# Kernel optimization log

Hardware: AMD Instinct MI355X
Metric: run time of the kernel (lower is better)

The kernel has to match this reference:

```python
import jax, jax.numpy as jnp
import numpy as np

B, N, E, H = 64, 2048, 256, 256


def _scan_dir(xproj, Whh, bhh, reverse):
    # xproj: (B, N, H) precomputed input projection; recurrence h_t = tanh(xproj_t + h @ Whh.T + bhh)
    def step(h, xt):
        h = jnp.tanh(xt + h @ Whh.T + bhh)
        return h, h
    h0 = jnp.zeros((xproj.shape[0], Whh.shape[0]), xproj.dtype)
    _, seq = jax.lax.scan(step, h0, jnp.swapaxes(xproj, 0, 1), reverse=reverse)
    return jnp.swapaxes(seq, 0, 1)  # (B, N, H)


def _bilayer(inp, Wf, bf, Uf, cf, Wb, bb, Ub, cb):
    fore = _scan_dir(inp @ Wf.T + bf, Uf, cf, False)
    back = _scan_dir(inp @ Wb.T + bb, Ub, cb, True)
    return jnp.concatenate([fore, back], axis=-1), fore[:, -1, :], back[:, 0, :]


def setup_inputs() -> dict:
    key = jax.random.key(0)
    ks = jax.random.split(key, 17)
    s_e = 1.0 / np.sqrt(E)
    s_h = 1.0 / np.sqrt(H)
    s_2h = 1.0 / np.sqrt(2 * H)
    f32 = jnp.float32
    return {
        'x': jax.random.normal(ks[0], (B, N, E), f32),
        'Wih_f0': jax.random.normal(ks[1], (H, E), f32) * s_e,
        'bih_f0': jax.random.normal(ks[2], (H,), f32) * s_e,
        'Whh_f0': jax.random.normal(ks[3], (H, H), f32) * s_h,
        'bhh_f0': jax.random.normal(ks[4], (H,), f32) * s_h,
        'Wih_b0': jax.random.normal(ks[5], (H, E), f32) * s_e,
        'bih_b0': jax.random.normal(ks[6], (H,), f32) * s_e,
        'Whh_b0': jax.random.normal(ks[7], (H, H), f32) * s_h,
        'bhh_b0': jax.random.normal(ks[8], (H,), f32) * s_h,
        'Wih_f1': jax.random.normal(ks[9], (H, 2 * H), f32) * s_2h,
        'bih_f1': jax.random.normal(ks[10], (H,), f32) * s_2h,
        'Whh_f1': jax.random.normal(ks[11], (H, H), f32) * s_h,
        'bhh_f1': jax.random.normal(ks[12], (H,), f32) * s_h,
        'Wih_b1': jax.random.normal(ks[13], (H, 2 * H), f32) * s_2h,
        'bih_b1': jax.random.normal(ks[14], (H,), f32) * s_2h,
        'Whh_b1': jax.random.normal(ks[15], (H, H), f32) * s_h,
        'bhh_b1': jax.random.normal(ks[16], (H,), f32) * s_h,
    }


def reference(x, Wih_f0, bih_f0, Whh_f0, bhh_f0, Wih_b0, bih_b0, Whh_b0, bhh_b0,
              Wih_f1, bih_f1, Whh_f1, bhh_f1, Wih_b1, bih_b1, Whh_b1, bhh_b1):
    out0, _, _ = _bilayer(x, Wih_f0, bih_f0, Whh_f0, bhh_f0, Wih_b0, bih_b0, Whh_b0, bhh_b0)
    _, h_f, h_b = _bilayer(out0, Wih_f1, bih_f1, Whh_f1, bhh_f1, Wih_b1, bih_b1, Whh_b1, bhh_b1)
    return jnp.concatenate([h_f, h_b], axis=-1)  # (B, 2H) final hidden of last layer
```

## Files before the change

### kernel.cpp

```cpp
#include <hip/hip_runtime.h>

#define BATCH 64
#define SEQ   2048
#define EIN   256
#define HID   256

typedef _Float16 f16;
typedef _Float16 f16x8 __attribute__((ext_vector_type(8)));
typedef float    f32x4 __attribute__((ext_vector_type(4)));

__global__ __launch_bounds__(256) void cast_f32_f16(
    const float* __restrict__ s, f16* __restrict__ d, int n)
{
    int i = (blockIdx.x * 256 + threadIdx.x) * 8;
    if (i >= n) return;
    const float4* sp = reinterpret_cast<const float4*>(s + i);
    float4 a = sp[0], b = sp[1];
    f16x8 v = { (f16)a.x, (f16)a.y, (f16)a.z, (f16)a.w,
                (f16)b.x, (f16)b.y, (f16)b.z, (f16)b.w };
    *reinterpret_cast<f16x8*>(d + i) = v;
}

__global__ __launch_bounds__(256, 2) void gemm_proj(
    const f16* __restrict__ A, const f16* __restrict__ W,
    const float* __restrict__ bias, f16* __restrict__ C, int K)
{
    const int tid  = threadIdx.x;
    const int wave = tid >> 6, lane = tid & 63;
    const int g    = lane >> 4, lr = lane & 15;
    const int bm   = blockIdx.x * 128;
    const int bn   = blockIdx.y * 128;
    const int wm   = (wave >> 1) * 64, wn = (wave & 1) * 64;

    __shared__ __align__(16) f16 As[128][72];
    __shared__ __align__(16) f16 Bs[128][72];

    f32x4 acc[4][4] = {};

    for (int kt = 0; kt < K; kt += 64) {
        __syncthreads();
#pragma unroll
        for (int i = 0; i < 4; ++i) {
            int c = i * 256 + tid;
            int r = c >> 3, sg = c & 7;
            *reinterpret_cast<f16x8*>(&As[r][sg * 8]) =
                *reinterpret_cast<const f16x8*>(A + (size_t)(bm + r) * K + kt + sg * 8);
            *reinterpret_cast<f16x8*>(&Bs[r][sg * 8]) =
                *reinterpret_cast<const f16x8*>(W + (size_t)(bn + r) * K + kt + sg * 8);
        }
        __syncthreads();
#pragma unroll
        for (int kf = 0; kf < 2; ++kf) {
            f16x8 af[4], bf[4];
#pragma unroll
            for (int f = 0; f < 4; ++f) {
                af[f] = *reinterpret_cast<const f16x8*>(&As[wm + f * 16 + lr][kf * 32 + g * 8]);
                bf[f] = *reinterpret_cast<const f16x8*>(&Bs[wn + f * 16 + lr][kf * 32 + g * 8]);
            }
#pragma unroll
            for (int fm = 0; fm < 4; ++fm)
#pragma unroll
                for (int fn = 0; fn < 4; ++fn)
                    acc[fm][fn] = __builtin_amdgcn_mfma_f32_16x16x32_f16(
                        af[fm], bf[fn], acc[fm][fn], 0, 0, 0);
        }
    }

#pragma unroll
    for (int fn = 0; fn < 4; ++fn) {
        float bv = bias[bn + wn + fn * 16 + lr];
#pragma unroll
        for (int fm = 0; fm < 4; ++fm) {
#pragma unroll
            for (int i = 0; i < 4; ++i) {
                int row = bm + wm + fm * 16 + g * 4 + i;
                int col = bn + wn + fn * 16 + lr;
                C[(size_t)row * 256 + col] = (f16)(acc[fm][fn][i] + bv);
            }
        }
    }
}

template<bool WRITE_SEQ>
__global__ __launch_bounds__(256, 1) void rnn_scan(
    const f16* __restrict__ xpF, const f16* __restrict__ xpB,
    const float* __restrict__ WhhF, const float* __restrict__ bhhF,
    const float* __restrict__ WhhB, const float* __restrict__ bhhB,
    f16* __restrict__ seq_out,
    float* __restrict__ fin_out)
{
    const int blk = blockIdx.x;
    const int b   = blk >> 1, dir = blk & 1;
    const f16*   xp  = dir ? xpB : xpF;
    const float* Whh = dir ? WhhB : WhhF;
    const float* bhh = dir ? bhhB : bhhF;

    const int tid  = threadIdx.x;
    const int wave = tid >> 6, lane = tid & 63;
    const int g    = lane >> 4, lr = lane & 15;
    const int n0   = wave * 64;

    __shared__ __align__(16) f16 hbuf[2][256];

    int kfj[8];
#pragma unroll
    for (int j = 0; j < 8; ++j) kfj[j] = (2 * wave + j) & 7;

    f16x8 wf[4][8];
#pragma unroll
    for (int fn = 0; fn < 4; ++fn) {
        const float* wr = Whh + (size_t)(n0 + fn * 16 + lr) * 256;
#pragma unroll
        for (int j = 0; j < 8; ++j) {
            const float4* p = reinterpret_cast<const float4*>(wr + kfj[j] * 32 + g * 8);
            float4 x0 = p[0], x1 = p[1];
            wf[fn][j] = (f16x8){ (f16)x0.x, (f16)x0.y, (f16)x0.z, (f16)x0.w,
                                 (f16)x1.x, (f16)x1.y, (f16)x1.z, (f16)x1.w };
        }
    }
    const float bv = bhh[tid];

    int aoff[8];
#pragma unroll
    for (int j = 0; j < 8; ++j) aoff[j] = kfj[j] * 64 + g * 16;
    char* lds0 = (char*)&hbuf[0][0];
    char* lds1 = (char*)&hbuf[1][0];

    hbuf[0][tid] = (f16)0.f;
    __syncthreads();

    const long long xstep = dir ? -256 : 256;
    const f16* xpre;
    {
        const f16* xptr = xp + (long long)b * SEQ * 256
                             + (long long)(dir ? SEQ - 1 : 0) * 256 + tid;
        xpre = xptr;
    }
    const long long sstep = dir ? -512 : 512;
    f16* sptr = nullptr;
    if (WRITE_SEQ)
        sptr = seq_out + ((long long)b * SEQ + (dir ? SEQ - 1 : 0)) * 512 + dir * 256 + tid;

    f16 ring[4];
#pragma unroll
    for (int r = 0; r < 3; ++r) { ring[r] = *xpre; xpre += xstep; }

    const f32x4 zf = {0.f, 0.f, 0.f, 0.f};
    float last_h = 0.f;

    f16x8 af[8];
    af[0] = *reinterpret_cast<const f16x8*>(lds0 + aoff[0]);
    af[1] = *reinterpret_cast<const f16x8*>(lds0 + aoff[1]);

    for (int s4 = 0; s4 < SEQ; s4 += 4) {
#pragma unroll
        for (int u = 0; u < 4; ++u) {
            char* cur = (u & 1) ? lds1 : lds0;
            char* nxt = (u & 1) ? lds0 : lds1;

#pragma unroll
            for (int j = 2; j < 8; ++j)
                af[j] = *reinterpret_cast<const f16x8*>(cur + aoff[j]);

            ring[(u + 3) & 3] = *xpre;
            xpre += xstep;

            f32x4 acc[4];
#pragma unroll
            for (int fn = 0; fn < 4; ++fn)
                acc[fn] = __builtin_amdgcn_mfma_f32_16x16x32_f16(af[0], wf[fn][0], zf, 0, 0, 0);
#pragma unroll
            for (int j = 1; j < 8; ++j)
#pragma unroll
                for (int fn = 0; fn < 4; ++fn)
                    acc[fn] = __builtin_amdgcn_mfma_f32_16x16x32_f16(af[j], wf[fn][j], acc[fn], 0, 0, 0);

            float r01 = (g & 1) ? acc[1][0] : acc[0][0];
            float r23 = (g & 1) ? acc[3][0] : acc[2][0];
            float mv  = (g & 2) ? r23 : r01;

            float pre = mv + (float)ring[u & 3] + bv;
            float e  = __builtin_exp2f(pre * 2.885390082f);
            float h  = 1.0f - 2.0f * __builtin_amdgcn_rcpf(e + 1.0f);
            f16 hh   = (f16)h;
            last_h   = h;

            *reinterpret_cast<f16*>(nxt + tid * 2) = hh;

            if (WRITE_SEQ) {
                *sptr = hh;
                sptr += sstep;
            }

            asm volatile("s_waitcnt lgkmcnt(0)" ::: "memory");
            af[0] = *reinterpret_cast<const f16x8*>(nxt + aoff[0]);
            af[1] = *reinterpret_cast<const f16x8*>(nxt + aoff[1]);

            __builtin_amdgcn_s_barrier();
            asm volatile("" ::: "memory");
        }
    }

    if (!WRITE_SEQ)
        fin_out[b * 512 + dir * 256 + tid] = last_h;
}

extern "C" void kernel_launch(void* const* d_in, const int* in_sizes, int n_in,
                              void* d_out, int out_size, void* d_ws, size_t ws_size,
                              hipStream_t stream)
{
    (void)in_sizes; (void)n_in; (void)out_size; (void)ws_size;

    const float* x      = (const float*)d_in[0];
    const float* Wih_f0 = (const float*)d_in[1];
    const float* bih_f0 = (const float*)d_in[2];
    const float* Whh_f0 = (const float*)d_in[3];
    const float* bhh_f0 = (const float*)d_in[4];
    const float* Wih_b0 = (const float*)d_in[5];
    const float* bih_b0 = (const float*)d_in[6];
    const float* Whh_b0 = (const float*)d_in[7];
    const float* bhh_b0 = (const float*)d_in[8];
    const float* Wih_f1 = (const float*)d_in[9];
    const float* bih_f1 = (const float*)d_in[10];
    const float* Whh_f1 = (const float*)d_in[11];
    const float* bhh_f1 = (const float*)d_in[12];
    const float* Wih_b1 = (const float*)d_in[13];
    const float* bih_b1 = (const float*)d_in[14];
    const float* Whh_b1 = (const float*)d_in[15];
    const float* bhh_b1 = (const float*)d_in[16];

    float* out = (float*)d_out;
    char*  ws  = (char*)d_ws;

    f16* xpF  = (f16*)(ws);
    f16* xpB  = (f16*)(ws + 67108864);
    f16* out0 = (f16*)(ws + 134217728);
    f16* x16  = (f16*)(ws + 268435456);
    f16* wf0  = (f16*)(ws + 335544320);
    f16* wb0  = (f16*)(ws + 335544320 + 131072);
    f16* wf1  = (f16*)(ws + 335544320 + 262144);
    f16* wb1  = (f16*)(ws + 335544320 + 524288);

    cast_f32_f16<<<16384, 256, 0, stream>>>(x, x16, 33554432);
    cast_f32_f16<<<32,    256, 0, stream>>>(Wih_f0, wf0, 65536);
    cast_f32_f16<<<32,    256, 0, stream>>>(Wih_b0, wb0, 65536);
    cast_f32_f16<<<64,    256, 0, stream>>>(Wih_f1, wf1, 131072);
    cast_f32_f16<<<64,    256, 0, stream>>>(Wih_b1, wb1, 131072);

    gemm_proj<<<dim3(1024, 2), 256, 0, stream>>>(x16, wf0, bih_f0, xpF, 256);
    gemm_proj<<<dim3(1024, 2), 256, 0, stream>>>(x16, wb0, bih_b0, xpB, 256);

    rnn_scan<true><<<128, 256, 0, stream>>>(xpF, xpB, Whh_f0, bhh_f0, Whh_b0, bhh_b0,
                                            out0, nullptr);

    gemm_proj<<<dim3(1024, 2), 256, 0, stream>>>(out0, wf1, bih_f1, xpF, 512);
    gemm_proj<<<dim3(1024, 2), 256, 0, stream>>>(out0, wb1, bih_b1, xpB, 512);

    rnn_scan<false><<<128, 256, 0, stream>>>(xpF, xpB, Whh_f1, bhh_f1, Whh_b1, bhh_b1,
                                             nullptr, out);
}
```

Before: 1.870 ms.

## Replace MFMA recurrent matvec with per-thread fdot2 dot products

The recurrent h@Whh^T step in the scan kernel no longer uses MFMA tiles. Each thread now holds its own full row of Whh as 128 packed f16x2 registers and computes its output with 128 v_dot2 instructions. It reads the whole 256-element hidden vector from LDS as broadcast f16x8 loads. This drops the MFMA latency chain and the fragment shuffling, but it adds far more VALU work per step, heavy register pressure, and 32 LDS broadcast reads per thread per step.

```diff
diff --git a/kernel.cpp b/kernel.cpp
--- a/kernel.cpp
+++ b/kernel.cpp
@@ -6,8 +6,17 @@
 #define HID   256
 
 typedef _Float16 f16;
+typedef _Float16 f16x2 __attribute__((ext_vector_type(2)));
 typedef _Float16 f16x8 __attribute__((ext_vector_type(8)));
 typedef float    f32x4 __attribute__((ext_vector_type(4)));
+
+__device__ __forceinline__ float dot2(f16x2 a, f16x2 b, float c) {
+#if __has_builtin(__builtin_amdgcn_fdot2)
+    return __builtin_amdgcn_fdot2(a, b, c, false);
+#else
+    return c + (float)a[0] * (float)b[0] + (float)a[1] * (float)b[1];
+#endif
+}
 
 __global__ __launch_bounds__(256) void cast_f32_f16(
     const float* __restrict__ s, f16* __restrict__ d, int n)
@@ -95,47 +104,28 @@
     const float* Whh = dir ? WhhB : WhhF;
     const float* bhh = dir ? bhhB : bhhF;
 
-    const int tid  = threadIdx.x;
-    const int wave = tid >> 6, lane = tid & 63;
-    const int g    = lane >> 4, lr = lane & 15;
-    const int n0   = wave * 64;
+    const int tid = threadIdx.x;
 
     __shared__ __align__(16) f16 hbuf[2][256];
 
-    int kfj[8];
-#pragma unroll
-    for (int j = 0; j < 8; ++j) kfj[j] = (2 * wave + j) & 7;
-
-    f16x8 wf[4][8];
-#pragma unroll
-    for (int fn = 0; fn < 4; ++fn) {
-        const float* wr = Whh + (size_t)(n0 + fn * 16 + lr) * 256;
-#pragma unroll
-        for (int j = 0; j < 8; ++j) {
-            const float4* p = reinterpret_cast<const float4*>(wr + kfj[j] * 32 + g * 8);
-            float4 x0 = p[0], x1 = p[1];
-            wf[fn][j] = (f16x8){ (f16)x0.x, (f16)x0.y, (f16)x0.z, (f16)x0.w,
-                                 (f16)x1.x, (f16)x1.y, (f16)x1.z, (f16)x1.w };
+    f16x2 w[128];
+    {
+        const float4* wr4 = reinterpret_cast<const float4*>(Whh + (size_t)tid * 256);
+#pragma unroll
+        for (int q = 0; q < 64; ++q) {
+            float4 v = wr4[q];
+            w[2 * q]     = (f16x2){ (f16)v.x, (f16)v.y };
+            w[2 * q + 1] = (f16x2){ (f16)v.z, (f16)v.w };
         }
     }
     const float bv = bhh[tid];
-
-    int aoff[8];
-#pragma unroll
-    for (int j = 0; j < 8; ++j) aoff[j] = kfj[j] * 64 + g * 16;
-    char* lds0 = (char*)&hbuf[0][0];
-    char* lds1 = (char*)&hbuf[1][0];
 
     hbuf[0][tid] = (f16)0.f;
     __syncthreads();
 
     const long long xstep = dir ? -256 : 256;
-    const f16* xpre;
-    {
-        const f16* xptr = xp + (long long)b * SEQ * 256
-                             + (long long)(dir ? SEQ - 1 : 0) * 256 + tid;
-        xpre = xptr;
-    }
+    const f16* xpre = xp + (long long)b * SEQ * 256
+                         + (long long)(dir ? SEQ - 1 : 0) * 256 + tid;
     const long long sstep = dir ? -512 : 512;
     f16* sptr = nullptr;
     if (WRITE_SEQ)
@@ -145,47 +135,71 @@
 #pragma unroll
     for (int r = 0; r < 3; ++r) { ring[r] = *xpre; xpre += xstep; }
 
-    const f32x4 zf = {0.f, 0.f, 0.f, 0.f};
     float last_h = 0.f;
 
-    f16x8 af[8];
-    af[0] = *reinterpret_cast<const f16x8*>(lds0 + aoff[0]);
-    af[1] = *reinterpret_cast<const f16x8*>(lds0 + aoff[1]);
-
     for (int s4 = 0; s4 < SEQ; s4 += 4) {
 #pragma unroll
         for (int u = 0; u < 4; ++u) {
-            char* cur = (u & 1) ? lds1 : lds0;
-            char* nxt = (u & 1) ? lds0 : lds1;
-
-#pragma unroll
-            for (int j = 2; j < 8; ++j)
-                af[j] = *reinterpret_cast<const f16x8*>(cur + aoff[j]);
+            const f16x8* hb8 = reinterpret_cast<const f16x8*>(
+                (u & 1) ? &hbuf[1][0] : &hbuf[0][0]);
+            f16* nxt = (u & 1) ? &hbuf[0][0] : &hbuf[1][0];
+
+            f16x8 bA[8], bB[8], bC[8];
+#pragma unroll
+            for (int r = 0; r < 8; ++r) bA[r] = hb8[r];
+#pragma unroll
+            for (int r = 0; r < 8; ++r) bB[r] = hb8[8 + r];
 
             ring[(u + 3) & 3] = *xpre;
             xpre += xstep;
 
-            f32x4 acc[4];
-#pragma unroll
-            for (int fn = 0; fn < 4; ++fn)
-                acc[fn] = __builtin_amdgcn_mfma_f32_16x16x32_f16(af[0], wf[fn][0], zf, 0, 0, 0);
-#pragma unroll
-            for (int j = 1; j < 8; ++j)
-#pragma unroll
-                for (int fn = 0; fn < 4; ++fn)
-                    acc[fn] = __builtin_amdgcn_mfma_f32_16x16x32_f16(af[j], wf[fn][j], acc[fn], 0, 0, 0);
-
-            float r01 = (g & 1) ? acc[1][0] : acc[0][0];
-            float r23 = (g & 1) ? acc[3][0] : acc[2][0];
-            float mv  = (g & 2) ? r23 : r01;
-
+            float a0 = 0.f, a1 = 0.f, a2 = 0.f, a3 = 0.f;
+
+#pragma unroll
+            for (int r = 0; r < 8; ++r) bC[r] = hb8[16 + r];
+#pragma unroll
+            for (int r = 0; r < 8; ++r) {
+                const f16x2* pp = reinterpret_cast<const f16x2*>(&bA[r]);
+                a0 = dot2(pp[0], w[r * 4 + 0], a0);
+                a1 = dot2(pp[1], w[r * 4 + 1], a1);
+                a2 = dot2(pp[2], w[r * 4 + 2], a2);
+                a3 = dot2(pp[3], w[r * 4 + 3], a3);
+            }
+#pragma unroll
+            for (int r = 0; r < 8; ++r) bA[r] = hb8[24 + r];
+#pragma unroll
+            for (int r = 0; r < 8; ++r) {
+                const f16x2* pp = reinterpret_cast<const f16x2*>(&bB[r]);
+                a0 = dot2(pp[0], w[32 + r * 4 + 0], a0);
+                a1 = dot2(pp[1], w[32 + r * 4 + 1], a1);
+                a2 = dot2(pp[2], w[32 + r * 4 + 2], a2);
+                a3 = dot2(pp[3], w[32 + r * 4 + 3], a3);
+            }
+#pragma unroll
+            for (int r = 0; r < 8; ++r) {
+                const f16x2* pp = reinterpret_cast<const f16x2*>(&bC[r]);
+                a0 = dot2(pp[0], w[64 + r * 4 + 0], a0);
+                a1 = dot2(pp[1], w[64 + r * 4 + 1], a1);
+                a2 = dot2(pp[2], w[64 + r * 4 + 2], a2);
+                a3 = dot2(pp[3], w[64 + r * 4 + 3], a3);
+            }
+#pragma unroll
+            for (int r = 0; r < 8; ++r) {
+                const f16x2* pp = reinterpret_cast<const f16x2*>(&bA[r]);
+                a0 = dot2(pp[0], w[96 + r * 4 + 0], a0);
+                a1 = dot2(pp[1], w[96 + r * 4 + 1], a1);
+                a2 = dot2(pp[2], w[96 + r * 4 + 2], a2);
+                a3 = dot2(pp[3], w[96 + r * 4 + 3], a3);
+            }
+
+            float mv  = (a0 + a1) + (a2 + a3);
             float pre = mv + (float)ring[u & 3] + bv;
             float e  = __builtin_exp2f(pre * 2.885390082f);
             float h  = 1.0f - 2.0f * __builtin_amdgcn_rcpf(e + 1.0f);
             f16 hh   = (f16)h;
             last_h   = h;
 
-            *reinterpret_cast<f16*>(nxt + tid * 2) = hh;
+            nxt[tid] = hh;
 
             if (WRITE_SEQ) {
                 *sptr = hh;
@@ -193,9 +207,6 @@
             }
 
             asm volatile("s_waitcnt lgkmcnt(0)" ::: "memory");
-            af[0] = *reinterpret_cast<const f16x8*>(nxt + aoff[0]);
-            af[1] = *reinterpret_cast<const f16x8*>(nxt + aoff[1]);
-
             __builtin_amdgcn_s_barrier();
             asm volatile("" ::: "memory");
         }
```

After: 2.646 ms. 41.5% more time.
